# Optimization experiments

Hardware: AMD Instinct MI355X
Metric: run time of the kernel (lower is better)

The kernel has to match this reference:

```python
import jax, jax.numpy as jnp
import numpy as np
from jax import lax

B, T, C, F = 64, 1152, 64, 8
L_DP, N_DP = 24, 12
NUM_CLASSES = 4


def setup_inputs() -> dict:
    key = jax.random.key(0)
    ks = jax.random.split(key, 8)
    num_chunks = T // L_DP
    return {
        "L_norm": jax.random.normal(ks[0], (B, C, C), jnp.float32) / C,
        "X_seq": jax.random.normal(ks[1], (B, T, C, F), jnp.float32),
        "deterministic": 1,
        "conv_kernel": jax.random.normal(ks[2], (32, 1, F, 8), jnp.float32) * 0.06,  # HWIO
        "ln_scale": jnp.ones((8,), jnp.float32),
        "ln_bias": jnp.zeros((8,), jnp.float32),
        "spatial_w": jax.random.normal(ks[3], (64, 4), jnp.float32) * 0.17,
        "W1": jax.random.normal(ks[4], (num_chunks * 64, 32), jnp.float32) * 0.02,
        "b1": jnp.zeros((32,), jnp.float32),
        "W2": jax.random.normal(ks[5], (32, NUM_CLASSES), jnp.float32) * 0.1,
        "b2": jnp.zeros((NUM_CLASSES,), jnp.float32),
    }


def _spike(x):
    return jnp.where(x > 0, 1.0, 0.0).astype(x.dtype)


def reference(L_norm, X_seq, deterministic, conv_kernel, ln_scale, ln_bias,
              spatial_w, W1, b1, W2, b2):
    # temporal conv over (T, C) spatial dims, F -> 8 channels, SAME padding
    ann = lax.conv_general_dilated(
        X_seq, conv_kernel, window_strides=(1, 1), padding="SAME",
        dimension_numbers=("NHWC", "HWIO", "NHWC"))
    # LayerNorm over last (feature) axis, eps=1e-6 (flax default)
    mu = jnp.mean(ann, axis=-1, keepdims=True)
    var = jnp.mean(jnp.square(ann - mu), axis=-1, keepdims=True)
    ann = (ann - mu) * lax.rsqrt(var + 1e-6) * ln_scale + ln_bias
    ann = jax.nn.relu(ann)
    # graph propagation + channel-spatial projection
    gx = jnp.einsum("bnm,btmf->btnf", L_norm, ann)          # (B,T,64,8)
    gx_csp = jnp.einsum("btcf,cs->btsf", gx, spatial_w)     # (B,T,4,8)
    snn_in = gx_csp.reshape(B, T, 32)

    # two-layer LIF recurrence over time (strictly sequential)
    def step(carry, x_t):
        mem1, mem2, mem_out = carry
        mem1 = mem1 * 0.8 + x_t
        spk1 = _spike(mem1 - 0.5)
        mem1 = mem1 - spk1 * 0.5
        mem2 = mem2 * 0.9 + spk1
        spk2 = _spike(mem2 - 0.5)
        mem2 = mem2 - spk2 * 0.5
        mem_out = mem_out * 0.95 + spk2
        return (mem1, mem2, mem_out), (mem_out, spk1, spk2)

    mem0 = jnp.zeros((B, 32), snn_in.dtype)
    _, (pot, spk1, spk2) = lax.scan(step, (mem0, mem0, mem0),
                                    jnp.swapaxes(snn_in, 0, 1))
    pot = jnp.swapaxes(pot, 0, 1)                           # (B,T,32)

    chunks = pot.reshape(B, T // L_DP, L_DP, 32)
    start_mean = jnp.mean(chunks[:, :, :N_DP, :], axis=2)
    end_mean = jnp.mean(chunks[:, :, -N_DP:, :], axis=2)
    flat = jnp.concatenate([start_mean, end_mean], axis=-1).reshape(B, -1)

    y = jax.nn.gelu(flat @ W1 + b1)   # flax nn.gelu default approximate=True
    logits = y @ W2 + b2
    firing_rate = (jnp.mean(spk1) + jnp.mean(spk2)) / 2.0
    return logits, firing_rate
```

## Files before the change

kernel.cpp:

```cpp
#include <hip/hip_runtime.h>
#include <hip/hip_fp16.h>
#include <math.h>

#define T_SEQ 1152

typedef _Float16 f16x8 __attribute__((ext_vector_type(8)));
typedef float f32x4 __attribute__((ext_vector_type(4)));

__global__ void mKernel(const float* __restrict__ L, const float* __restrict__ sw,
                        float* __restrict__ Mbuf) {
  int b = blockIdx.x, tid = threadIdx.x;
  int s = tid >> 6, m = tid & 63;
  float a = 0.f;
  #pragma unroll 4
  for (int n = 0; n < 64; ++n)
    a = fmaf(sw[n * 4 + s], L[(b * 64 + n) * 64 + m], a);
  Mbuf[b * 256 + m * 4 + s] = a;
}

__global__ __launch_bounds__(256, 4)
void convKernel(const float* __restrict__ X, const float* __restrict__ Kw,
                const float* __restrict__ lnS, const float* __restrict__ lnB,
                const float* __restrict__ Mbuf, float* __restrict__ snn) {
  __shared__ int4   XS[8 * 65];
  __shared__ float4 hT4[512];

  const int bid  = blockIdx.x;
  const int b    = bid / 36;
  const int tile = bid - b * 36;
  const int t0   = tile * 32;
  const int tid  = threadIdx.x;
  const int lane = tid & 63;
  const int wid  = tid >> 6;
  const int tcol = lane & 15;
  const int rg   = lane >> 4;
  const int fq   = rg & 1;
  const int tloc = tcol + ((rg >> 1) << 4);

  const int rA = lane & 15;
  const int fr = rA & 7;
  const int sh16 = (rA >> 3) << 4;
  f16x8 ka[12];
  #pragma unroll
  for (int q = 0; q < 12; ++q) {
    const int khs = 4 * q + rg - sh16;
    #pragma unroll
    for (int j = 0; j < 8; ++j) {
      float kv = (khs >= 0 && khs < 32) ? Kw[khs * 64 + j * 8 + fr] : 0.f;
      ka[q][j] = (_Float16)kv;
    }
  }

  const int tpt   = lane >> 1;
  const int cslot = lane & 1;

  const int sc2 = tid & 7;
  const int srow0 = tid >> 3;
  const int srow1 = srow0 + 32;
  const int st0 = t0 - 15 + srow0;
  const int st1 = t0 - 15 + srow1;
  const bool v0 = (st0 >= 0) && (st0 < T_SEQ);
  const bool v1 = (srow1 < 63) && (st1 >= 0) && (st1 < T_SEQ);
  const float* xb = X + (size_t)(b * T_SEQ) * 512;

  float pacc[4][8];
  #pragma unroll
  for (int s = 0; s < 4; ++s)
    #pragma unroll
    for (int f = 0; f < 8; ++f) pacc[s][f] = 0.f;

  #pragma unroll 1
  for (int part = 0; part < 8; ++part) {
    {
      const float* xp = xb + (part * 8 + sc2) * 8;
      float4 a0 = make_float4(0.f, 0.f, 0.f, 0.f), a1 = a0;
      float4 b0 = a0, b1 = a0;
      if (v0) { const float* p = xp + (size_t)st0 * 512; a0 = *(const float4*)p; a1 = *(const float4*)(p + 4); }
      if (v1) { const float* p = xp + (size_t)st1 * 512; b0 = *(const float4*)p; b1 = *(const float4*)(p + 4); }
      {
        unsigned u0 = __builtin_bit_cast(unsigned, __float22half2_rn(make_float2(a0.x, a0.y)));
        unsigned u1 = __builtin_bit_cast(unsigned, __float22half2_rn(make_float2(a0.z, a0.w)));
        unsigned u2 = __builtin_bit_cast(unsigned, __float22half2_rn(make_float2(a1.x, a1.y)));
        unsigned u3 = __builtin_bit_cast(unsigned, __float22half2_rn(make_float2(a1.z, a1.w)));
        int4 v; v.x = (int)u0; v.y = (int)u1; v.z = (int)u2; v.w = (int)u3;
        XS[sc2 * 65 + srow0] = v;
      }
      if (srow1 < 63) {
        unsigned u0 = __builtin_bit_cast(unsigned, __float22half2_rn(make_float2(b0.x, b0.y)));
        unsigned u1 = __builtin_bit_cast(unsigned, __float22half2_rn(make_float2(b0.z, b0.w)));
        unsigned u2 = __builtin_bit_cast(unsigned, __float22half2_rn(make_float2(b1.x, b1.y)));
        unsigned u3 = __builtin_bit_cast(unsigned, __float22half2_rn(make_float2(b1.z, b1.w)));
        int4 v; v.x = (int)u0; v.y = (int)u1; v.z = (int)u2; v.w = (int)u3;
        XS[sc2 * 65 + srow1] = v;
      }
    }
    __syncthreads();

    #pragma unroll
    for (int cp = 0; cp < 2; ++cp) {
      f32x4 acc = {0.f, 0.f, 0.f, 0.f};
      const int rb = (wid * 2 + cp) * 65 + tcol + rg;
      #pragma unroll
      for (int q = 0; q < 12; ++q) {
        f16x8 xf = __builtin_bit_cast(f16x8, XS[rb + 4 * q]);
        acc = __builtin_amdgcn_mfma_f32_16x16x32_f16(ka[q], xf, acc, 0, 0, 0);
      }
      float4 st; st.x = acc[0]; st.y = acc[1]; st.z = acc[2]; st.w = acc[3];
      hT4[wid * 128 + cp * 64 + fq * 32 + tloc] = st;
    }

    {
      float4 lo = hT4[wid * 128 + cslot * 64 + tpt];
      float4 hi = hT4[wid * 128 + cslot * 64 + 32 + tpt];
      float hv[8] = { lo.x, lo.y, lo.z, lo.w, hi.x, hi.y, hi.z, hi.w };
      float mu = 0.f;
      #pragma unroll
      for (int f = 0; f < 8; ++f) mu += hv[f];
      mu *= 0.125f;
      float var = 0.f;
      #pragma unroll
      for (int f = 0; f < 8; ++f) { float d = hv[f] - mu; hv[f] = d; var = fmaf(d, d, var); }
      float rs = 1.0f / sqrtf(var * 0.125f + 1e-6f);
      const int c = part * 8 + wid * 2 + cslot;
      const float4 Mc = *(const float4*)(Mbuf + b * 256 + c * 4);
      #pragma unroll
      for (int f = 0; f < 8; ++f) {
        float hh = fmaxf(fmaf(hv[f] * rs, lnS[f], lnB[f]), 0.f);
        pacc[0][f] = fmaf(hh, Mc.x, pacc[0][f]);
        pacc[1][f] = fmaf(hh, Mc.y, pacc[1][f]);
        pacc[2][f] = fmaf(hh, Mc.z, pacc[2][f]);
        pacc[3][f] = fmaf(hh, Mc.w, pacc[3][f]);
      }
    }
    __syncthreads();
  }

  #pragma unroll
  for (int s = 0; s < 4; ++s)
    #pragma unroll
    for (int f = 0; f < 8; ++f)
      pacc[s][f] += __shfl_xor(pacc[s][f], 1, 64);

  float* R = (float*)hT4;
  #pragma unroll
  for (int pass = 0; pass < 2; ++pass) {
    __syncthreads();
    if (wid > 0 && cslot == 0) {
      #pragma unroll
      for (int s2 = 0; s2 < 2; ++s2)
        #pragma unroll
        for (int f = 0; f < 8; ++f)
          R[((wid - 1) * 32 + tpt) * 16 + s2 * 8 + f] = pacc[pass * 2 + s2][f];
    }
    __syncthreads();
    if (wid == 0 && cslot == 0) {
      float* op = snn + ((size_t)b * T_SEQ + t0 + tpt) * 32;
      #pragma unroll
      for (int s2 = 0; s2 < 2; ++s2) {
        const int s = pass * 2 + s2;
        float v[8];
        #pragma unroll
        for (int f = 0; f < 8; ++f)
          v[f] = pacc[s][f]
               + R[(0 * 32 + tpt) * 16 + s2 * 8 + f]
               + R[(1 * 32 + tpt) * 16 + s2 * 8 + f]
               + R[(2 * 32 + tpt) * 16 + s2 * 8 + f];
        *(float4*)(op + s * 8)     = make_float4(v[0], v[1], v[2], v[3]);
        *(float4*)(op + s * 8 + 4) = make_float4(v[4], v[5], v[6], v[7]);
      }
    }
  }
}

__global__ __launch_bounds__(64, 1)
void scanKernel(const float* __restrict__ snn, float* __restrict__ flat,
                float* __restrict__ spkPart) {
  const int tid = threadIdx.x;
  const int j = tid & 31;
  const int b = blockIdx.x * 2 + (tid >> 5);
  const float* base = snn + (size_t)b * T_SEQ * 32 + j;

  float m1 = 0.f, m2 = 0.f, mo = 0.f, s1 = 0.f, s2 = 0.f;
  float cur[24], nxt[24];
  #pragma unroll
  for (int u = 0; u < 24; ++u) cur[u] = base[(size_t)u * 32];

  #pragma unroll 1
  for (int ch = 0; ch < 48; ++ch) {
    if (ch < 47) {
      #pragma unroll
      for (int u = 0; u < 24; ++u) nxt[u] = base[(size_t)((ch + 1) * 24 + u) * 32];
    }
    float aS = 0.f, aE = 0.f;
    #pragma unroll
    for (int u = 0; u < 24; ++u) {
      m1 = m1 * 0.8f + cur[u];
      float sp1 = (m1 > 0.5f) ? 1.f : 0.f;  m1 -= sp1 * 0.5f;
      m2 = m2 * 0.9f + sp1;
      float sp2 = (m2 > 0.5f) ? 1.f : 0.f;  m2 -= sp2 * 0.5f;
      mo = mo * 0.95f + sp2;
      s1 += sp1; s2 += sp2;
      if (u < 12) aS += mo; else aE += mo;
    }
    flat[b * 3072 + ch * 64 + j]      = aS / 12.0f;
    flat[b * 3072 + ch * 64 + 32 + j] = aE / 12.0f;
    if (ch < 47) {
      #pragma unroll
      for (int u = 0; u < 24; ++u) cur[u] = nxt[u];
    }
  }
  for (int off = 16; off > 0; off >>= 1) {
    s1 += __shfl_down(s1, off, 32);
    s2 += __shfl_down(s2, off, 32);
  }
  if (j == 0) { spkPart[b * 2] = s1; spkPart[b * 2 + 1] = s2; }
}

__global__ void mlpKernel(const float* __restrict__ flat, const float* __restrict__ W1,
                          const float* __restrict__ b1, const float* __restrict__ W2,
                          const float* __restrict__ b2, const float* __restrict__ spkPart,
                          float* __restrict__ out) {
  if (blockIdx.x == 64) {
    if (threadIdx.x == 0) {
      float s1 = 0.f, s2 = 0.f;
      for (int i = 0; i < 64; ++i) { s1 += spkPart[2*i]; s2 += spkPart[2*i+1]; }
      out[256] = (s1 + s2) * 0.5f / (64.0f * 1152.0f * 32.0f);
    }
    return;
  }
  const int b = blockIdx.x;
  const int tid = threadIdx.x;
  const int u = tid & 31, kc = tid >> 5;
  __shared__ float red[256];
  __shared__ float ys[32];
  float p = 0.f;
  const int kbeg = kc * 384, kend = kbeg + 384;
  #pragma unroll 4
  for (int k = kbeg; k < kend; ++k)
    p = fmaf(flat[b*3072 + k], W1[k*32 + u], p);
  red[tid] = p;
  __syncthreads();
  if (kc == 0) {
    float y = b1[u];
    #pragma unroll
    for (int q = 0; q < 8; ++q) y += red[q*32 + u];
    float y3 = y * y * y;
    float th = tanhf(0.7978845608028654f * (y + 0.044715f * y3));
    ys[u] = 0.5f * y * (1.0f + th);
  }
  __syncthreads();
  if (tid < 4) {
    float accv = b2[tid];
    #pragma unroll
    for (int q = 0; q < 32; ++q) accv = fmaf(ys[q], W2[q*4 + tid], accv);
    out[b*4 + tid] = accv;
  }
}

extern "C" void kernel_launch(void* const* d_in, const int* in_sizes, int n_in,
                              void* d_out, int out_size, void* d_ws, size_t ws_size,
                              hipStream_t stream) {
  const float* L   = (const float*)d_in[0];
  const float* X   = (const float*)d_in[1];
  const float* Kw  = (const float*)d_in[3];
  const float* lnS = (const float*)d_in[4];
  const float* lnB = (const float*)d_in[5];
  const float* sw  = (const float*)d_in[6];
  const float* W1  = (const float*)d_in[7];
  const float* b1  = (const float*)d_in[8];
  const float* W2  = (const float*)d_in[9];
  const float* b2  = (const float*)d_in[10];

  float* ws   = (float*)d_ws;
  float* Mbuf = ws;
  float* snn  = Mbuf + 16384;
  float* flat = snn + 2359296;
  float* spk  = flat + 196608;
  float* out  = (float*)d_out;

  mKernel<<<64, 256, 0, stream>>>(L, sw, Mbuf);
  convKernel<<<2304, 256, 0, stream>>>(X, Kw, lnS, lnB, Mbuf, snn);
  scanKernel<<<32, 64, 0, stream>>>(snn, flat, spk);
  mlpKernel<<<65, 256, 0, stream>>>(flat, W1, b1, W2, b2, spk, out);
}
```

Baseline: 149.8 us.

## Double-buffer conv input tile and prefetch next channel part during MFMA

```diff
diff --git a/kernel.cpp b/kernel.cpp
--- a/kernel.cpp
+++ b/kernel.cpp
@@ -22,7 +22,7 @@
 void convKernel(const float* __restrict__ X, const float* __restrict__ Kw,
                 const float* __restrict__ lnS, const float* __restrict__ lnB,
                 const float* __restrict__ Mbuf, float* __restrict__ snn) {
-  __shared__ int4   XS[8 * 65];
+  __shared__ int4   XS[2][8 * 65];
   __shared__ float4 hT4[512];
 
   const int bid  = blockIdx.x;
@@ -69,40 +69,52 @@
     #pragma unroll
     for (int f = 0; f < 8; ++f) pacc[s][f] = 0.f;
 
+  const float4 z4 = make_float4(0.f, 0.f, 0.f, 0.f);
+
+#define CVT_WRITE(BUF, P0, P1, Q0, Q1)                                       \
+  { {                                                                        \
+      unsigned u0 = __builtin_bit_cast(unsigned, __float22half2_rn(make_float2(P0.x, P0.y))); \
+      unsigned u1 = __builtin_bit_cast(unsigned, __float22half2_rn(make_float2(P0.z, P0.w))); \
+      unsigned u2 = __builtin_bit_cast(unsigned, __float22half2_rn(make_float2(P1.x, P1.y))); \
+      unsigned u3 = __builtin_bit_cast(unsigned, __float22half2_rn(make_float2(P1.z, P1.w))); \
+      int4 v; v.x = (int)u0; v.y = (int)u1; v.z = (int)u2; v.w = (int)u3;    \
+      XS[BUF][sc2 * 65 + srow0] = v;                                         \
+    }                                                                        \
+    if (srow1 < 63) {                                                        \
+      unsigned u0 = __builtin_bit_cast(unsigned, __float22half2_rn(make_float2(Q0.x, Q0.y))); \
+      unsigned u1 = __builtin_bit_cast(unsigned, __float22half2_rn(make_float2(Q0.z, Q0.w))); \
+      unsigned u2 = __builtin_bit_cast(unsigned, __float22half2_rn(make_float2(Q1.x, Q1.y))); \
+      unsigned u3 = __builtin_bit_cast(unsigned, __float22half2_rn(make_float2(Q1.z, Q1.w))); \
+      int4 v; v.x = (int)u0; v.y = (int)u1; v.z = (int)u2; v.w = (int)u3;    \
+      XS[BUF][sc2 * 65 + srow1] = v;                                         \
+    } }
+
+  {
+    const float* xp = xb + sc2 * 8;
+    float4 a0 = z4, a1 = z4, b0 = z4, b1 = z4;
+    if (v0) { const float* p = xp + (size_t)st0 * 512; a0 = *(const float4*)p; a1 = *(const float4*)(p + 4); }
+    if (v1) { const float* p = xp + (size_t)st1 * 512; b0 = *(const float4*)p; b1 = *(const float4*)(p + 4); }
+    CVT_WRITE(0, a0, a1, b0, b1)
+  }
+  __syncthreads();
+
   #pragma unroll 1
   for (int part = 0; part < 8; ++part) {
-    {
-      const float* xp = xb + (part * 8 + sc2) * 8;
-      float4 a0 = make_float4(0.f, 0.f, 0.f, 0.f), a1 = a0;
-      float4 b0 = a0, b1 = a0;
-      if (v0) { const float* p = xp + (size_t)st0 * 512; a0 = *(const float4*)p; a1 = *(const float4*)(p + 4); }
-      if (v1) { const float* p = xp + (size_t)st1 * 512; b0 = *(const float4*)p; b1 = *(const float4*)(p + 4); }
-      {
-        unsigned u0 = __builtin_bit_cast(unsigned, __float22half2_rn(make_float2(a0.x, a0.y)));
-        unsigned u1 = __builtin_bit_cast(unsigned, __float22half2_rn(make_float2(a0.z, a0.w)));
-        unsigned u2 = __builtin_bit_cast(unsigned, __float22half2_rn(make_float2(a1.x, a1.y)));
-        unsigned u3 = __builtin_bit_cast(unsigned, __float22half2_rn(make_float2(a1.z, a1.w)));
-        int4 v; v.x = (int)u0; v.y = (int)u1; v.z = (int)u2; v.w = (int)u3;
-        XS[sc2 * 65 + srow0] = v;
-      }
-      if (srow1 < 63) {
-        unsigned u0 = __builtin_bit_cast(unsigned, __float22half2_rn(make_float2(b0.x, b0.y)));
-        unsigned u1 = __builtin_bit_cast(unsigned, __float22half2_rn(make_float2(b0.z, b0.w)));
-        unsigned u2 = __builtin_bit_cast(unsigned, __float22half2_rn(make_float2(b1.x, b1.y)));
-        unsigned u3 = __builtin_bit_cast(unsigned, __float22half2_rn(make_float2(b1.z, b1.w)));
-        int4 v; v.x = (int)u0; v.y = (int)u1; v.z = (int)u2; v.w = (int)u3;
-        XS[sc2 * 65 + srow1] = v;
-      }
-    }
-    __syncthreads();
-
+    float4 pa0 = z4, pa1 = z4, pb0 = z4, pb1 = z4;
+    if (part < 7) {
+      const float* xp = xb + ((part + 1) * 8 + sc2) * 8;
+      if (v0) { const float* p = xp + (size_t)st0 * 512; pa0 = *(const float4*)p; pa1 = *(const float4*)(p + 4); }
+      if (v1) { const float* p = xp + (size_t)st1 * 512; pb0 = *(const float4*)p; pb1 = *(const float4*)(p + 4); }
+    }
+
+    const int4* xsb = XS[part & 1];
     #pragma unroll
     for (int cp = 0; cp < 2; ++cp) {
       f32x4 acc = {0.f, 0.f, 0.f, 0.f};
       const int rb = (wid * 2 + cp) * 65 + tcol + rg;
       #pragma unroll
       for (int q = 0; q < 12; ++q) {
-        f16x8 xf = __builtin_bit_cast(f16x8, XS[rb + 4 * q]);
+        f16x8 xf = __builtin_bit_cast(f16x8, xsb[rb + 4 * q]);
         acc = __builtin_amdgcn_mfma_f32_16x16x32_f16(ka[q], xf, acc, 0, 0, 0);
       }
       float4 st; st.x = acc[0]; st.y = acc[1]; st.z = acc[2]; st.w = acc[3];
@@ -132,8 +144,13 @@
         pacc[3][f] = fmaf(hh, Mc.w, pacc[3][f]);
       }
     }
+
+    if (part < 7) {
+      CVT_WRITE((part + 1) & 1, pa0, pa1, pb0, pb1)
+    }
     __syncthreads();
   }
+#undef CVT_WRITE
 
   #pragma unroll
   for (int s = 0; s < 4; ++s)
```

After: 148.3 us. No clear change (-1.0%).
